# Kernel optimization log

Measured on AMD Instinct MI355X. Metric: run time of the kernel, lower is better.

## Reference

```python
import jax, jax.numpy as jnp
import numpy as np

N_NODES, N_EDGES, N_GRAPHS = 8192, 32768, 256
FXD, HEADS = 78, 10
D2 = FXD * HEADS  # 780
FF = 2048
L_MUT = 735
NF = 32
OUT_DIM = 128


def _ln(x, g, b, eps=1e-5):
    m = x.mean(-1, keepdims=True)
    v = ((x - m) ** 2).mean(-1, keepdims=True)
    return (x - m) * jax.lax.rsqrt(v + eps) * g + b


def _transformer(x, in_w, in_b, out_w, out_b, ln1_g, ln1_b, l1_w, l1_b, l2_w, l2_b, ln2_g, ln2_b):
    # post-LN TransformerEncoderLayer, nhead=1, seq = all N nodes, batch = 1 (eval: dropout off)
    E = x.shape[-1]
    q, k, v = jnp.split(x @ in_w.T + in_b, 3, axis=-1)
    a = jax.nn.softmax((q @ k.T) * (1.0 / np.sqrt(E)), axis=-1) @ v  # [N,N] scores
    x = _ln(x + a @ out_w.T + out_b, ln1_g, ln1_b)
    h = jax.nn.relu(x @ l1_w.T + l1_b) @ l2_w.T + l2_b
    return _ln(x + h, ln2_g, ln2_b)


def _gat(x, src, dst, w, a_src, a_dst, bias):
    # PyG GATConv, heads=10, concat=True, leaky 0.2, self loops already in src/dst
    N = x.shape[0]
    h = (x @ w.T).reshape(N, HEADS, FXD)
    asrc = (h * a_src).sum(-1)  # [N,H]
    adst = (h * a_dst).sum(-1)
    alpha = jax.nn.leaky_relu(asrc[src] + adst[dst], 0.2)  # [E,H]
    amax = jax.lax.stop_gradient(jax.ops.segment_max(alpha, dst, num_segments=N))
    ex = jnp.exp(alpha - amax[dst])
    coef = ex / (jax.ops.segment_sum(ex, dst, num_segments=N)[dst] + 1e-16)
    out = jax.ops.segment_sum(coef[:, :, None] * h[src], dst, num_segments=N)
    return out.reshape(N, HEADS * FXD) + bias


def _gcn(x, src, dst, w, b):
    # PyG GCNConv with self loops (already in src/dst), symmetric norm
    N = x.shape[0]
    deg = jax.ops.segment_sum(jnp.ones(dst.shape, x.dtype), dst, num_segments=N)
    dis = jnp.where(deg > 0, jax.lax.rsqrt(jnp.maximum(deg, 1.0)), 0.0)
    norm = dis[src] * dis[dst]
    return jax.ops.segment_sum(norm[:, None] * (x @ w.T)[src], dst, num_segments=N) + b


def _conv1d(x, w, b):
    y = jax.lax.conv_general_dilated(x, w, (1,), 'VALID', dimension_numbers=('NCH', 'OIH', 'NCH'))
    return y + b[None, :, None]


def _convT1d(x, w, b):
    # torch ConvTranspose1d weight [in,out,k] -> flipped [out,in,k], full padding
    k = w.shape[-1]
    ker = jnp.flip(w, -1).transpose(1, 0, 2)
    y = jax.lax.conv_general_dilated(x, ker, (1,), [(k - 1, k - 1)], dimension_numbers=('NCH', 'OIH', 'NCH'))
    return y + b[None, :, None]


def _maxpool1d(x, k):
    return jax.lax.reduce_window(x, -jnp.inf, jax.lax.max, (1, 1, k), (1, 1, k), 'VALID')


def _bn_eval(x, g, b, eps=1e-5):
    # eval-mode BatchNorm1d with fresh running stats (mean 0, var 1)
    return x * (g / np.sqrt(1.0 + eps))[None, :, None] + b[None, :, None]


def _forward(edge_index, batch, x, target_mut, t1_in_w, t1_in_b, t1_out_w, t1_out_b, t1_ln1_g, t1_ln1_b, t1_l1_w, t1_l1_b, t1_l2_w, t1_l2_b, t1_ln2_g, t1_ln2_b, gat_w, gat_asrc, gat_adst, gat_b, t2_in_w, t2_in_b, t2_out_w, t2_out_b, t2_ln1_g, t2_ln1_b, t2_l1_w, t2_l1_b, t2_l2_w, t2_l2_b, t2_ln2_g, t2_ln2_b, gcn_w, gcn_b, fcg1_w, fcg1_b, fcg2_w, fcg2_b, e1_w, e1_b, bn1_g, bn1_b, e2_w, e2_b, bn2_g, bn2_b, e3_w, e3_b, enc_lin_w, enc_lin_b, d3_w, d3_b, dbn2_g, dbn2_b, d2_w, d2_b, dbn1_g, dbn1_b, d1_w, d1_b, fc1_w, fc1_b, fc2_w, fc2_b, out_w, out_b):
    N = x.shape[0]
    xg = _transformer(x, t1_in_w, t1_in_b, t1_out_w, t1_out_b, t1_ln1_g, t1_ln1_b, t1_l1_w, t1_l1_b, t1_l2_w, t1_l2_b, t1_ln2_g, t1_ln2_b)
    loops = jnp.arange(N, dtype=edge_index.dtype)
    src = jnp.concatenate([edge_index[0], loops])
    dst = jnp.concatenate([edge_index[1], loops])
    xg = jax.nn.relu(_gat(xg, src, dst, gat_w, gat_asrc, gat_adst, gat_b))
    xg = _transformer(xg, t2_in_w, t2_in_b, t2_out_w, t2_out_b, t2_ln1_g, t2_ln1_b, t2_l1_w, t2_l1_b, t2_l2_w, t2_l2_b, t2_ln2_g, t2_ln2_b)
    xg = jax.nn.relu(_gcn(xg, src, dst, gcn_w, gcn_b))
    gm = jax.ops.segment_max(xg, batch, num_segments=N_GRAPHS)
    gm = jnp.where(jnp.isfinite(gm), gm, 0.0)
    cnt = jax.ops.segment_sum(jnp.ones((N,), xg.dtype), batch, num_segments=N_GRAPHS)
    ga = jax.ops.segment_sum(xg, batch, num_segments=N_GRAPHS) / jnp.maximum(cnt, 1.0)[:, None]
    xd = jnp.concatenate([gm, ga], axis=1)  # [B, 1560]
    xd = jax.nn.relu(xd @ fcg1_w.T + fcg1_b)
    xd = xd @ fcg2_w.T + fcg2_b  # [B, 128]
    # conv1d autoencoder on mutation profile
    t = target_mut[:, None, :]  # [B,1,735]
    e = jax.nn.leaky_relu(_bn_eval(_maxpool1d(_conv1d(t, e1_w, e1_b), 8), bn1_g, bn1_b))
    e = jax.nn.leaky_relu(_bn_eval(_maxpool1d(_conv1d(e, e2_w, e2_b), 7), bn2_g, bn2_b))
    e = _conv1d(e, e3_w, e3_b)  # [B,128,5]
    z = e.reshape(e.shape[0], -1) @ enc_lin_w.T + enc_lin_b  # [B,128]
    d = jnp.repeat(jax.nn.leaky_relu(_bn_eval(_convT1d(e, d3_w, d3_b), dbn2_g, dbn2_b)), 7, axis=-1)
    d = jnp.repeat(jax.nn.leaky_relu(_bn_eval(_convT1d(d, d2_w, d2_b), dbn1_g, dbn1_b)), 8, axis=-1)
    decode = _convT1d(d, d1_w, d1_b)  # [B,1,735]
    xc = jnp.concatenate([xd, z], axis=1)
    xc = jax.nn.relu(xc @ fc1_w.T + fc1_b)
    xc = jax.nn.relu(xc @ fc2_w.T + fc2_b)
    out = jax.nn.sigmoid(xc @ out_w.T + out_b)
    return (out, xd, decode)


def setup_inputs():
    key = jax.random.key(0)
    ks = iter(jax.random.split(key, 64))

    def rn(*shape):
        return jax.random.normal(next(ks), shape, jnp.float32) * 0.05

    inp = {}
    inp['x'] = jax.random.normal(next(ks), (N_NODES, FXD), jnp.float32)
    inp['edge_index'] = jax.random.randint(next(ks), (2, N_EDGES), 0, N_NODES)
    inp['batch'] = jnp.sort(jax.random.randint(next(ks), (N_NODES,), 0, N_GRAPHS))
    inp['target_mut'] = jax.random.normal(next(ks), (N_GRAPHS, L_MUT), jnp.float32)
    for p, E in (('t1', FXD), ('t2', D2)):
        inp[p + '_in_w'] = rn(3 * E, E); inp[p + '_in_b'] = jnp.zeros((3 * E,))
        inp[p + '_out_w'] = rn(E, E); inp[p + '_out_b'] = jnp.zeros((E,))
        inp[p + '_ln1_g'] = jnp.ones((E,)); inp[p + '_ln1_b'] = jnp.zeros((E,))
        inp[p + '_l1_w'] = rn(FF, E); inp[p + '_l1_b'] = jnp.zeros((FF,))
        inp[p + '_l2_w'] = rn(E, FF); inp[p + '_l2_b'] = jnp.zeros((E,))
        inp[p + '_ln2_g'] = jnp.ones((E,)); inp[p + '_ln2_b'] = jnp.zeros((E,))
    inp['gat_w'] = rn(D2, FXD); inp['gat_asrc'] = rn(HEADS, FXD); inp['gat_adst'] = rn(HEADS, FXD); inp['gat_b'] = jnp.zeros((D2,))
    inp['gcn_w'] = rn(D2, D2); inp['gcn_b'] = jnp.zeros((D2,))
    inp['fcg1_w'] = rn(1500, 2 * D2); inp['fcg1_b'] = jnp.zeros((1500,))
    inp['fcg2_w'] = rn(OUT_DIM, 1500); inp['fcg2_b'] = jnp.zeros((OUT_DIM,))
    inp['e1_w'] = rn(NF, 1, 8); inp['e1_b'] = jnp.zeros((NF,))
    inp['bn1_g'] = jnp.ones((NF,)); inp['bn1_b'] = jnp.zeros((NF,))
    inp['e2_w'] = rn(2 * NF, NF, 8); inp['e2_b'] = jnp.zeros((2 * NF,))
    inp['bn2_g'] = jnp.ones((2 * NF,)); inp['bn2_b'] = jnp.zeros((2 * NF,))
    inp['e3_w'] = rn(4 * NF, 2 * NF, 8); inp['e3_b'] = jnp.zeros((4 * NF,))
    inp['enc_lin_w'] = rn(OUT_DIM, 640); inp['enc_lin_b'] = jnp.zeros((OUT_DIM,))
    inp['d3_w'] = rn(4 * NF, 2 * NF, 8); inp['d3_b'] = jnp.zeros((2 * NF,))
    inp['dbn2_g'] = jnp.ones((2 * NF,)); inp['dbn2_b'] = jnp.zeros((2 * NF,))
    inp['d2_w'] = rn(2 * NF, NF, 8); inp['d2_b'] = jnp.zeros((NF,))
    inp['dbn1_g'] = jnp.ones((NF,)); inp['dbn1_b'] = jnp.zeros((NF,))
    inp['d1_w'] = rn(NF, 1, 8); inp['d1_b'] = jnp.zeros((1,))
    inp['fc1_w'] = rn(1024, 2 * OUT_DIM); inp['fc1_b'] = jnp.zeros((1024,))
    inp['fc2_w'] = rn(128, 1024); inp['fc2_b'] = jnp.zeros((128,))
    inp['out_w'] = rn(1, 128); inp['out_b'] = jnp.zeros((1,))
    return inp


def reference(x, edge_index, batch, target_mut, t1_in_w, t1_in_b, t1_out_w, t1_out_b, t1_ln1_g, t1_ln1_b, t1_l1_w, t1_l1_b, t1_l2_w, t1_l2_b, t1_ln2_g, t1_ln2_b, gat_w, gat_asrc, gat_adst, gat_b, t2_in_w, t2_in_b, t2_out_w, t2_out_b, t2_ln1_g, t2_ln1_b, t2_l1_w, t2_l1_b, t2_l2_w, t2_l2_b, t2_ln2_g, t2_ln2_b, gcn_w, gcn_b, fcg1_w, fcg1_b, fcg2_w, fcg2_b, e1_w, e1_b, bn1_g, bn1_b, e2_w, e2_b, bn2_g, bn2_b, e3_w, e3_b, enc_lin_w, enc_lin_b, d3_w, d3_b, dbn2_g, dbn2_b, d2_w, d2_b, dbn1_g, dbn1_b, d1_w, d1_b, fc1_w, fc1_b, fc2_w, fc2_b, out_w, out_b):
    return _forward(edge_index, batch, x, target_mut, t1_in_w, t1_in_b, t1_out_w, t1_out_b, t1_ln1_g, t1_ln1_b, t1_l1_w, t1_l1_b, t1_l2_w, t1_l2_b, t1_ln2_g, t1_ln2_b, gat_w, gat_asrc, gat_adst, gat_b, t2_in_w, t2_in_b, t2_out_w, t2_out_b, t2_ln1_g, t2_ln1_b, t2_l1_w, t2_l1_b, t2_l2_w, t2_l2_b, t2_ln2_g, t2_ln2_b, gcn_w, gcn_b, fcg1_w, fcg1_b, fcg2_w, fcg2_b, e1_w, e1_b, bn1_g, bn1_b, e2_w, e2_b, bn2_g, bn2_b, e3_w, e3_b, enc_lin_w, enc_lin_b, d3_w, d3_b, dbn2_g, dbn2_b, d2_w, d2_b, dbn1_g, dbn1_b, d1_w, d1_b, fc1_w, fc1_b, fc2_w, fc2_b, out_w, out_b)
```

## Files before the change

kernel.cpp:

```cpp
#include <hip/hip_runtime.h>
#include <math.h>

#define NN     8192
#define NEDGE  32768
#define NETOT  40960
#define NG     256
#define FXD_   78
#define NH     10
#define DD2    780
#define FFD    2048
#define LMUT   735

static inline int cdiv_i(long long a, int b){ return (int)((a + (long long)b - 1) / b); }
static inline int pad32(int x){ return (x + 31) & ~31; }

typedef __attribute__((ext_vector_type(8))) short bf16x8;
typedef __attribute__((ext_vector_type(4))) float f32x4;

static __device__ __forceinline__ unsigned short f2bf(float f){
    unsigned u = __float_as_uint(f);
    u += 0x7FFFu + ((u >> 16) & 1u);
    return (unsigned short)(u >> 16);
}

static __device__ __forceinline__ void gload16(const void* g, void* l){
    __builtin_amdgcn_global_load_lds((const __attribute__((address_space(1))) void*)g,
                                     (__attribute__((address_space(3))) void*)l, 16, 0, 0);
}

__global__ void fill_f32_k(float* __restrict__ p, float v, long long n){
    long long i = (long long)blockIdx.x * 256 + threadIdx.x;
    if (i < n) p[i] = v;
}
__global__ void fill_u32_k(unsigned* __restrict__ p, unsigned v, long long n){
    long long i = (long long)blockIdx.x * 256 + threadIdx.x;
    if (i < n) p[i] = v;
}

__global__ void cvt_pad_k(const float* __restrict__ src, unsigned short* __restrict__ dst,
                          long long n , int C, int lds_, int ldd)
{
    long long i = (long long)blockIdx.x * 256 + threadIdx.x;
    if (i >= n) return;
    int r = (int)(i / ldd), c = (int)(i % ldd);
    dst[i] = (c < C) ? f2bf(src[(size_t)r * lds_ + c]) : (unsigned short)0;
}

__global__ void tr_bf16_k(const unsigned short* __restrict__ src, unsigned short* __restrict__ dst,
                          int R, int C, int lds_, int ldd)
{
    __shared__ unsigned short t[32][33];
    int cb = blockIdx.x * 32, rb = blockIdx.y * 32;
    int tx = threadIdx.x & 31, ty = threadIdx.x >> 5;
#pragma unroll
    for (int i = 0; i < 4; ++i){
        int r = rb + ty + i * 8, c = cb + tx;
        t[ty + i * 8][tx] = (r < R && c < C) ? src[(size_t)r * lds_ + c] : (unsigned short)0;
    }
    __syncthreads();
#pragma unroll
    for (int i = 0; i < 4; ++i){
        int dr = cb + ty + i * 8, dc = rb + tx;
        if (dr < C && dc < R) dst[(size_t)dr * ldd + dc] = t[tx][ty + i * 8];
    }
}

__global__ void qkv_bias_k(const float* __restrict__ b3, float* __restrict__ out, int E, int Ep)
{
    int idx = blockIdx.x * 256 + threadIdx.x;
    if (idx >= 3 * Ep) return;
    int s = idx / Ep, c = idx % Ep;
    out[idx] = (c < E) ? b3[s * E + c] : 0.f;
}

__global__ void bias_add_k(float* __restrict__ X, const float* __restrict__ b, long long n, int cols)
{
    long long i = (long long)blockIdx.x * 256 + threadIdx.x;
    if (i < n) X[i] += b[i % cols];
}

template<int OUTC, int ACT, int SPLITK, int BROW, int BN>
__global__ __launch_bounds__(256) void mgemm_k(
    const unsigned short* __restrict__ A, const unsigned short* __restrict__ B,
    const float* __restrict__ bias, void* __restrict__ Cv,
    int M, int N, int Kp, int lda, int ldb, int ldc, int swz)
{
    constexpr int NFJ   = BN / 32;
    constexpr int TILEA = 128 * 32;
    constexpr int TILEB = BN * 32;
    __shared__ unsigned short As[2 * TILEA];
    __shared__ unsigned short Bs[2 * TILEB];
    const int tid = threadIdx.x;
    const int lane = tid & 63, wid = tid >> 6;
    const int r16 = lane & 15, q = lane >> 4;
    const int wr = (wid >> 1) * 64, wc = (wid & 1) * (BN / 2);

    const int gx = gridDim.x, gy = gridDim.y;
    const int nwg = gx * gy;
    int orig = swz ? ((int)blockIdx.x * gy + (int)blockIdx.y)
                   : ((int)blockIdx.y * gx + (int)blockIdx.x);
    int q8 = nwg >> 3, r8 = nwg & 7;
    int xcd = orig & 7, kk8 = orig >> 3;
    int wgid = (xcd < r8 ? xcd * (q8 + 1) : r8 * (q8 + 1) + (xcd - r8) * q8) + kk8;
    int bx, by;
    if (swz){ by = wgid % gy; bx = wgid / gy; }
    else    { bx = wgid % gx; by = wgid / gx; }
    const int row0 = by * 128, col0 = bx * BN;

    int kbeg = 0, kend = Kp;
    if (SPLITK > 1){
        int nt_ = Kp >> 5, cpt = (nt_ + SPLITK - 1) / SPLITK;
        kbeg = (int)blockIdx.z * cpt * 32;
        kend = min(Kp, kbeg + cpt * 32);
    }

    const int c0 = wid * 128 + lane;
    const int r0a = c0 >> 2, k0a = (c0 & 3) << 3;
    const size_t gA0 = (size_t)min(row0 + r0a, M - 1) * lda + k0a;
    const size_t gA1 = (size_t)min(row0 + r0a + 16, M - 1) * lda + k0a;
    unsigned short* lA = As + wid * 1024;
    size_t gB0 = 0, gB1 = 0;
    unsigned short* lB;
    if (BN == 128){
        gB0 = (size_t)min(col0 + r0a, N - 1) * ldb + k0a;
        gB1 = (size_t)min(col0 + r0a + 16, N - 1) * ldb + k0a;
        lB = Bs + wid * 1024;
    } else {
        const int cb = wid * 64 + lane;
        const int rb_ = cb >> 2, kb_ = (cb & 3) << 3;
        gB0 = (size_t)min(col0 + rb_, N - 1) * ldb + kb_;
        lB = Bs + wid * 512;
    }

    f32x4 acc[4][NFJ];
#pragma unroll
    for (int i = 0; i < 4; ++i)
#pragma unroll
        for (int j = 0; j < NFJ; ++j){ f32x4 z = {0.f, 0.f, 0.f, 0.f}; acc[i][j] = z; }

    const int nt = (kend - kbeg) >> 5;
    if (nt > 0){
        gload16(A + gA0 + kbeg, lA);
        gload16(A + gA1 + kbeg, lA + 512);
        gload16(B + gB0 + kbeg, lB);
        if (BN == 128) gload16(B + gB1 + kbeg, lB + 512);
        __syncthreads();
        int cur = 0;
        for (int t = 0; t < nt; ++t){
            const int k0 = kbeg + (t << 5);
            if (t + 1 < nt){
                const int kn = k0 + 32, nb = cur ^ 1;
                gload16(A + gA0 + kn, lA + nb * TILEA);
                gload16(A + gA1 + kn, lA + nb * TILEA + 512);
                gload16(B + gB0 + kn, lB + nb * TILEB);
                if (BN == 128) gload16(B + gB1 + kn, lB + nb * TILEB + 512);
            }
            const unsigned short* Ab = As + cur * TILEA;
            const unsigned short* Bb = Bs + cur * TILEB;
            bf16x8 af[4], bfv[NFJ];
#pragma unroll
            for (int f = 0; f < 4; ++f)
                af[f] = *(const bf16x8*)(Ab + (size_t)(wr + f * 16 + r16) * 32 + (q << 3));
#pragma unroll
            for (int f = 0; f < NFJ; ++f)
                bfv[f] = *(const bf16x8*)(Bb + (size_t)(wc + f * 16 + r16) * 32 + (q << 3));
#pragma unroll
            for (int fi = 0; fi < 4; ++fi)
#pragma unroll
                for (int fj = 0; fj < NFJ; ++fj)
                    acc[fi][fj] = __builtin_amdgcn_mfma_f32_16x16x32_bf16(af[fi], bfv[fj], acc[fi][fj], 0, 0, 0);
            __syncthreads();
            cur ^= 1;
        }
    }

#pragma unroll
    for (int fi = 0; fi < 4; ++fi){
#pragma unroll
        for (int j = 0; j < 4; ++j){
            int r = row0 + wr + fi * 16 + q * 4 + j;
            if (r >= M) continue;
#pragma unroll
            for (int fj = 0; fj < NFJ; ++fj){
                int c = col0 + wc + fj * 16 + r16;
                if (c >= N) continue;
                float v = acc[fi][fj][j];
                if (SPLITK > 1){
                    atomicAdd((float*)Cv + (size_t)r * ldc + c, v);
                } else {
                    if (bias) v += BROW ? bias[r] : bias[c];
                    if (ACT == 1) v = fmaxf(v, 0.f);
                    if (ACT == 2) v = 1.f / (1.f + expf(-v));
                    if (OUTC == 0) ((float*)Cv)[(size_t)r * ldc + c] = v;
                    else ((unsigned short*)Cv)[(size_t)r * ldc + c] = f2bf(v);
                }
            }
        }
    }
}

template<int OUTC, int ACT, int SPLITK, int BROW, int BN>
static void mgemm(hipStream_t s, const unsigned short* A, const unsigned short* B,
                  const float* bias, void* C, int M, int N, int Kp,
                  int lda, int ldb, int ldc, int swz)
{
    dim3 g(cdiv_i(N, BN), cdiv_i(M, 128), SPLITK);
    mgemm_k<OUTC, ACT, SPLITK, BROW, BN><<<g, 256, 0, s>>>(A, B, bias, C, M, N, Kp, lda, ldb, ldc, swz);
}

__global__ __launch_bounds__(256) void softmax_bf16_k(unsigned short* __restrict__ SP, float scale)
{
    __shared__ float red[8];
    const int tid = threadIdx.x;
    uint4* prow = (uint4*)(SP + (size_t)blockIdx.x * NN);
    float v[32];
    float mx = -3.4e38f;
#pragma unroll
    for (int c = 0; c < 4; ++c){
        uint4 t = prow[c * 256 + tid];
        const unsigned* u = (const unsigned*)&t;
#pragma unroll
        for (int j = 0; j < 4; ++j){
            float lo = __uint_as_float(u[j] << 16) * scale;
            float hi = __uint_as_float(u[j] & 0xFFFF0000u) * scale;
            v[c * 8 + j * 2]     = lo;
            v[c * 8 + j * 2 + 1] = hi;
            mx = fmaxf(mx, fmaxf(lo, hi));
        }
    }
#pragma unroll
    for (int off = 32; off; off >>= 1) mx = fmaxf(mx, __shfl_xor(mx, off, 64));
    if ((tid & 63) == 0) red[tid >> 6] = mx;
    __syncthreads();
    mx = fmaxf(fmaxf(red[0], red[1]), fmaxf(red[2], red[3]));
    float sum = 0.f;
#pragma unroll
    for (int i = 0; i < 32; ++i){ v[i] = expf(v[i] - mx); sum += v[i]; }
#pragma unroll
    for (int off = 32; off; off >>= 1) sum += __shfl_xor(sum, off, 64);
    if ((tid & 63) == 0) red[4 + (tid >> 6)] = sum;
    __syncthreads();
    float inv = 1.f / (red[4] + red[5] + red[6] + red[7]);
#pragma unroll
    for (int c = 0; c < 4; ++c){
        uint4 t;
        unsigned* u = (unsigned*)&t;
#pragma unroll
        for (int j = 0; j < 4; ++j){
            unsigned lo = f2bf(v[c * 8 + j * 2] * inv);
            unsigned hi = f2bf(v[c * 8 + j * 2 + 1] * inv);
            u[j] = lo | (hi << 16);
        }
        prow[c * 256 + tid] = t;
    }
}

__global__ __launch_bounds__(256) void add_ln_k(
    const float* __restrict__ X, const float* __restrict__ Y, const float* __restrict__ ybias,
    const float* __restrict__ g, const float* __restrict__ b,
    float* __restrict__ out, unsigned short* __restrict__ obf, int E, int Ep)
{
    __shared__ float s1[256], s2[256];
    const int tid = threadIdx.x;
    long long base = (long long)blockIdx.x * E;
    float vals[4];
    float sum = 0.f, sq = 0.f;
    int i = 0;
    for (int c = tid; c < Ep; c += 256, ++i){
        float v = 0.f;
        if (c < E){
            v = X[base + c] + Y[base + c];
            if (ybias) v += ybias[c];
            sum += v; sq += v * v;
        }
        vals[i] = v;
    }
    s1[tid] = sum; s2[tid] = sq; __syncthreads();
    for (int s = 128; s; s >>= 1){
        if (tid < s){ s1[tid] += s1[tid + s]; s2[tid] += s2[tid + s]; }
        __syncthreads();
    }
    float mean = s1[0] / (float)E;
    float var = s2[0] / (float)E - mean * mean;
    if (var < 0.f) var = 0.f;
    float inv = 1.f / sqrtf(var + 1e-5f);
    i = 0;
    for (int c = tid; c < Ep; c += 256, ++i){
        if (c < E){
            float o = (vals[i] - mean) * inv * g[c] + b[c];
            out[base + c] = o;
            if (obf) obf[(size_t)blockIdx.x * Ep + c] = f2bf(o);
        } else if (obf) obf[(size_t)blockIdx.x * Ep + c] = 0;
    }
}

static __device__ __forceinline__ unsigned enc_f(float x){
    unsigned u = __float_as_uint(x);
    return (u & 0x80000000u) ? ~u : (u | 0x80000000u);
}
static __device__ __forceinline__ float dec_f(unsigned u){
    return (u & 0x80000000u) ? __uint_as_float(u & 0x7fffffffu) : __uint_as_float(~u);
}
static __device__ __forceinline__ void edge_sd(const int* __restrict__ ei, int e, int& s, int& d){
    if (e < NEDGE){ s = ei[e]; d = ei[NEDGE + e]; }
    else { s = e - NEDGE; d = e - NEDGE; }
}

__global__ void gat_srcdst_k(const float* __restrict__ h, const float* __restrict__ aw_src,
                             const float* __restrict__ aw_dst, float* __restrict__ asrc,
                             float* __restrict__ adst)
{
    int idx = blockIdx.x * 256 + threadIdx.x;
    if (idx >= NN * NH) return;
    int n = idx / NH, hh = idx % NH;
    const float* hp = h + (long long)n * DD2 + hh * FXD_;
    const float* ws = aw_src + hh * FXD_;
    const float* wd = aw_dst + hh * FXD_;
    float s1 = 0.f, s2 = 0.f;
    for (int f = 0; f < FXD_; ++f){ float v = hp[f]; s1 += v * ws[f]; s2 += v * wd[f]; }
    asrc[idx] = s1; adst[idx] = s2;
}

__global__ void gat_alpha_k(const int* __restrict__ ei, const float* __restrict__ asrc,
                            const float* __restrict__ adst, float* __restrict__ alpha,
                            unsigned* __restrict__ amax)
{
    int idx = blockIdx.x * 256 + threadIdx.x;
    if (idx >= NETOT * NH) return;
    int e = idx / NH, hh = idx % NH;
    int s, d; edge_sd(ei, e, s, d);
    float a = asrc[s * NH + hh] + adst[d * NH + hh];
    a = (a > 0.f) ? a : 0.2f * a;
    alpha[idx] = a;
    atomicMax(&amax[d * NH + hh], enc_f(a));
}

__global__ void gat_expsum_k(const int* __restrict__ ei, float* __restrict__ alpha,
                             const unsigned* __restrict__ amax, float* __restrict__ denom)
{
    int idx = blockIdx.x * 256 + threadIdx.x;
    if (idx >= NETOT * NH) return;
    int e = idx / NH, hh = idx % NH;
    int s, d; edge_sd(ei, e, s, d);
    float m = dec_f(amax[d * NH + hh]);
    float ex = expf(alpha[idx] - m);
    alpha[idx] = ex;
    atomicAdd(&denom[d * NH + hh], ex);
}

__global__ void deg_count_k(const int* __restrict__ ei, int* __restrict__ deg)
{
    int e = blockIdx.x * 256 + threadIdx.x;
    if (e >= NETOT) return;
    int s, d; edge_sd(ei, e, s, d);
    atomicAdd(&deg[d], 1);
}

__global__ __launch_bounds__(256) void csr_off_k(const int* __restrict__ deg,
                                                 int* __restrict__ off, int* __restrict__ cur)
{
    __shared__ int pref[257];
    const int tid = threadIdx.x;
    int loc[32];
    int base = tid * 32, sum = 0;
#pragma unroll
    for (int i = 0; i < 32; ++i){ loc[i] = sum; sum += deg[base + i]; }
    __shared__ int part[256];
    part[tid] = sum; __syncthreads();
    if (tid == 0){
        pref[0] = 0;
        for (int i = 0; i < 256; ++i) pref[i + 1] = pref[i] + part[i];
    }
    __syncthreads();
    int p0 = pref[tid];
#pragma unroll
    for (int i = 0; i < 32; ++i){ off[base + i] = p0 + loc[i]; cur[base + i] = p0 + loc[i]; }
    if (tid == 0) off[NN] = pref[256];
}

__global__ void csr_fill_k(const int* __restrict__ ei, int* __restrict__ cur,
                           int* __restrict__ csr_s, int* __restrict__ csr_e)
{
    int e = blockIdx.x * 256 + threadIdx.x;
    if (e >= NETOT) return;
    int s, d; edge_sd(ei, e, s, d);
    int pos = atomicAdd(&cur[d], 1);
    csr_s[pos] = s; csr_e[pos] = e;
}

__global__ __launch_bounds__(256) void gat_gather_k(
    const int* __restrict__ off, const int* __restrict__ csr_s, const int* __restrict__ csr_e,
    const float* __restrict__ ex, const float* __restrict__ denom,
    const float* __restrict__ hfeat, float* __restrict__ out)
{
    const int d = blockIdx.x, tid = threadIdx.x;
    const int beg = off[d], end = off[d + 1];
    for (int f = tid; f < DD2; f += 256){
        int hh = f / FXD_;
        float acc = 0.f;
        for (int p = beg; p < end; ++p)
            acc += ex[csr_e[p] * NH + hh] * hfeat[(size_t)csr_s[p] * DD2 + f];
        out[(size_t)d * DD2 + f] = acc / (denom[d * NH + hh] + 1e-16f);
    }
}

__global__ __launch_bounds__(256) void gcn_gather_k(
    const int* __restrict__ off, const int* __restrict__ csr_s,
    const float* __restrict__ dis, const float* __restrict__ xw, float* __restrict__ out)
{
    const int d = blockIdx.x, tid = threadIdx.x;
    const int beg = off[d], end = off[d + 1];
    const float dd_ = dis[d];
    for (int f = tid; f < DD2; f += 256){
        float acc = 0.f;
        for (int p = beg; p < end; ++p){
            int s = csr_s[p];
            acc += dis[s] * xw[(size_t)s * DD2 + f];
        }
        out[(size_t)d * DD2 + f] = acc * dd_;
    }
}

__global__ void bias_relu_k(float* __restrict__ X, const float* __restrict__ b,
                            unsigned short* __restrict__ obf, int rows, int cols, int ldp)
{
    long long i = (long long)blockIdx.x * 256 + threadIdx.x;
    if (i >= (long long)rows * ldp) return;
    int r = (int)(i / ldp), c = (int)(i % ldp);
    if (c < cols){
        float v = X[(size_t)r * cols + c] + b[c];
        v = v > 0.f ? v : 0.f;
        X[(size_t)r * cols + c] = v;
        if (obf) obf[i] = f2bf(v);
    } else if (obf) obf[i] = 0;
}

__global__ void dis_k(const int* __restrict__ deg, float* __restrict__ dis)
{
    int n = blockIdx.x * 256 + threadIdx.x;
    if (n >= NN) return;
    float d = (float)deg[n];
    dis[n] = (d > 0.f) ? 1.f / sqrtf(fmaxf(d, 1.f)) : 0.f;
}

__global__ void seg_start_k(const int* __restrict__ batch, int* __restrict__ start)
{
    int n = blockIdx.x * 256 + threadIdx.x;
    if (n >= NN) return;
    int b = batch[n];
    int bp = (n == 0) ? -1 : batch[n - 1];
    for (int g = bp + 1; g <= b; ++g) start[g] = n;
    if (n == NN - 1){
        for (int g = b + 1; g <= NG; ++g) start[g] = NN;
    }
}

__global__ __launch_bounds__(256) void pool_seg_k(const float* __restrict__ xg,
                                                  const int* __restrict__ start,
                                                  unsigned short* __restrict__ xdb)
{
    const int g = blockIdx.x, tid = threadIdx.x;
    const int s0 = start[g], s1 = start[g + 1];
    const float inv = 1.f / fmaxf((float)(s1 - s0), 1.f);
    for (int f = tid; f < DD2; f += 256){
        float mx = 0.f, sm = 0.f;
        for (int n = s0; n < s1; ++n){
            float v = xg[(size_t)n * DD2 + f];
            mx = fmaxf(mx, v); sm += v;
        }
        xdb[(size_t)g * 1568 + f] = f2bf(mx);
        xdb[(size_t)g * 1568 + DD2 + f] = f2bf(sm * inv);
    }
    if (tid < 8) xdb[(size_t)g * 1568 + 1560 + tid] = 0;
}

#define BN_SCALE 0.9999950000374996f

__global__ __launch_bounds__(256) void enc1_b(const float* __restrict__ tm, const float* __restrict__ w,
                                              const float* __restrict__ bias, const float* __restrict__ bng,
                                              const float* __restrict__ bnb, float* __restrict__ out)
{
    __shared__ float xs[736];
    __shared__ float ws[256], bs[32], gs[32], b2[32];
    const int g = blockIdx.x, tid = threadIdx.x;
    for (int i = tid; i < 735; i += 256) xs[i] = tm[(size_t)g * LMUT + i];
    ws[tid] = w[tid];
    if (tid < 32){ bs[tid] = bias[tid]; gs[tid] = bng[tid]; b2[tid] = bnb[tid]; }
    __syncthreads();
    for (int idx = tid; idx < 32 * 91; idx += 256){
        int o = idx / 91, t = idx % 91;
        float mx = -3.4e38f;
        for (int p = 0; p < 8; ++p){
            float s = bs[o];
#pragma unroll
            for (int k = 0; k < 8; ++k) s += xs[t * 8 + p + k] * ws[o * 8 + k];
            mx = fmaxf(mx, s);
        }
        float v = mx * gs[o] * BN_SCALE + b2[o];
        out[(size_t)g * 2912 + idx] = v > 0.f ? v : 0.01f * v;
    }
}

__global__ void i2c_enc2_k(const float* __restrict__ in, unsigned short* __restrict__ A){
    int idx = blockIdx.x * 256 + threadIdx.x;
    if (idx >= NG * 84 * 256) return;
    int col = idx & 255, row = idx >> 8;
    int g = row / 84, u = row % 84;
    int i = col >> 3, k = col & 7;
    A[idx] = f2bf(in[(size_t)g * 2912 + i * 91 + u + k]);
}
__global__ void post_enc2_k(const float* __restrict__ G, const float* __restrict__ b,
                            const float* __restrict__ bng, const float* __restrict__ bnb,
                            float* __restrict__ out){
    int idx = blockIdx.x * 256 + threadIdx.x;
    if (idx >= NG * 768) return;
    int t = idx % 12, o = (idx / 12) & 63, g = idx / 768;
    float mx = -3.4e38f;
#pragma unroll
    for (int p = 0; p < 7; ++p) mx = fmaxf(mx, G[(size_t)(g * 84 + t * 7 + p) * 64 + o]);
    float v = (mx + b[o]) * bng[o] * BN_SCALE + bnb[o];
    out[(size_t)g * 768 + o * 12 + t] = v > 0.f ? v : 0.01f * v;
}
__global__ void i2c_enc3_k(const float* __restrict__ in, unsigned short* __restrict__ A){
    int idx = blockIdx.x * 256 + threadIdx.x;
    if (idx >= NG * 5 * 512) return;
    int col = idx & 511, row = idx >> 9;
    int g = row / 5, t = row % 5;
    int i2 = col >> 3, k = col & 7;
    A[idx] = f2bf(in[(size_t)g * 768 + i2 * 12 + t + k]);
}
__global__ void post_enc3_k(const float* __restrict__ G, const float* __restrict__ b,
                            float* __restrict__ e3o, unsigned short* __restrict__ obf){
    int idx = blockIdx.x * 256 + threadIdx.x;
    if (idx >= NG * 640) return;
    int t = idx % 5, o = (idx / 5) & 127, g = idx / 640;
    float v = G[(size_t)(g * 5 + t) * 128 + o] + b[o];
    e3o[(size_t)g * 640 + o * 5 + t] = v;
    obf[(size_t)g * 640 + o * 5 + t] = f2bf(v);
}
__global__ void wshuf_k(const float* __restrict__ src, unsigned short* __restrict__ dst, int I, int O){
    int idx = blockIdx.x * 256 + threadIdx.x;
    if (idx >= I * O * 8) return;
    int o = idx / (I * 8), rem = idx % (I * 8);
    int i = rem >> 3, j = rem & 7;
    dst[idx] = f2bf(src[(size_t)(i * O + o) * 8 + j]);
}
__global__ void i2c_dec3_k(const float* __restrict__ e3o, unsigned short* __restrict__ A){
    int idx = blockIdx.x * 256 + threadIdx.x;
    if (idx >= NG * 12 * 1024) return;
    int col = idx & 1023, row = idx >> 10;
    int g = row / 12, t = row % 12;
    int i2 = col >> 3, j = col & 7;
    int tt = t - j;
    A[idx] = (tt >= 0 && tt < 5) ? f2bf(e3o[(size_t)g * 640 + i2 * 5 + tt]) : (unsigned short)0;
}
__global__ void post_dec3_k(const float* __restrict__ G, const float* __restrict__ b,
                            const float* __restrict__ bng, const float* __restrict__ bnb,
                            float* __restrict__ dd3){
    int idx = blockIdx.x * 256 + threadIdx.x;
    if (idx >= NG * 768) return;
    int t = idx % 12, o = (idx / 12) & 63, g = idx / 768;
    float v = (G[(size_t)(g * 12 + t) * 64 + o] + b[o]) * bng[o] * BN_SCALE + bnb[o];
    dd3[(size_t)g * 768 + o * 12 + t] = v > 0.f ? v : 0.01f * v;
}
__global__ void i2c_dec2_k(const float* __restrict__ dd3, unsigned short* __restrict__ A){
    int idx = blockIdx.x * 256 + threadIdx.x;
    if (idx >= NG * 91 * 512) return;
    int col = idx & 511, row = idx >> 9;
    int g = row / 91, t = row % 91;
    int i2 = col >> 3, j = col & 7;
    int tt = t - j;
    A[idx] = (tt >= 0 && tt < 84) ? f2bf(dd3[(size_t)g * 768 + i2 * 12 + tt / 7]) : (unsigned short)0;
}
__global__ void post_dec2_k(const float* __restrict__ G, const float* __restrict__ b,
                            const float* __restrict__ bng, const float* __restrict__ bnb,
                            float* __restrict__ dd2){
    int idx = blockIdx.x * 256 + threadIdx.x;
    if (idx >= NG * 2912) return;
    int t = idx % 91, o = (idx / 91) & 31, g = idx / 2912;
    float v = (G[(size_t)(g * 91 + t) * 32 + o] + b[o]) * bng[o] * BN_SCALE + bnb[o];
    dd2[(size_t)g * 2912 + o * 91 + t] = v > 0.f ? v : 0.01f * v;
}

__global__ __launch_bounds__(256) void dec1_b(const float* __restrict__ dd2, const float* __restrict__ w,
                                              const float* __restrict__ bias, float* __restrict__ out)
{
    __shared__ float d2s[32][91];
    __shared__ float ws[256];
    const int g = blockIdx.x, tid = threadIdx.x;
    const int t0 = (int)blockIdx.y * 245;
    for (int i = tid; i < 32 * 91; i += 256) d2s[i / 91][i % 91] = dd2[(size_t)g * 2912 + i];
    ws[tid] = w[tid];
    __syncthreads();
    if (tid < 245){
        int t = t0 + tid;
        int id8[8]; bool ok[8];
#pragma unroll
        for (int j = 0; j < 8; ++j){
            int tt = t - j;
            ok[j] = (tt >= 0 && tt < 728);
            id8[j] = ok[j] ? (tt >> 3) : 0;
        }
        float s = bias[0];
        for (int i2 = 0; i2 < 32; ++i2){
            const float* wp = ws + i2 * 8;
            float a = 0.f;
#pragma unroll
            for (int j = 0; j < 8; ++j) if (ok[j]) a += d2s[i2][id8[j]] * wp[j];
            s += a;
        }
        out[(size_t)g * 735 + t] = s;
    }
}

__global__ void concat_xc_k(const float* __restrict__ xd, const float* __restrict__ z,
                            unsigned short* __restrict__ xcb)
{
    int idx = blockIdx.x * 256 + threadIdx.x;
    if (idx >= NG * 256) return;
    int g = idx >> 8, c = idx & 255;
    xcb[idx] = f2bf((c < 128) ? xd[g * 128 + c] : z[g * 128 + (c - 128)]);
}

extern "C" void kernel_launch(void* const* d_in, const int* in_sizes, int n_in,
                              void* d_out, int out_size, void* d_ws, size_t ws_size,
                              hipStream_t stream)
{
    (void)in_sizes; (void)n_in; (void)out_size;

    const float* x      = (const float*)d_in[0];
    const int*   ei     = (const int*)  d_in[1];
    const int*   batch  = (const int*)  d_in[2];
    const float* tmut   = (const float*)d_in[3];
    const float* t1w[12]; for (int i = 0; i < 12; ++i) t1w[i] = (const float*)d_in[4 + i];
    const float* t2w[12]; for (int i = 0; i < 12; ++i) t2w[i] = (const float*)d_in[16 + i];
    const float* gat_w    = (const float*)d_in[28];
    const float* gat_asrc = (const float*)d_in[29];
    const float* gat_adst = (const float*)d_in[30];
    const float* gat_b    = (const float*)d_in[31];
    const float* gcn_w  = (const float*)d_in[32];
    const float* gcn_b  = (const float*)d_in[33];
    const float* fcg1_w = (const float*)d_in[34];
    const float* fcg1_b = (const float*)d_in[35];
    const float* fcg2_w = (const float*)d_in[36];
    const float* fcg2_b = (const float*)d_in[37];
    const float* e1_w = (const float*)d_in[38]; const float* e1_b = (const float*)d_in[39];
    const float* bn1_g = (const float*)d_in[40]; const float* bn1_b = (const float*)d_in[41];
    const float* e2_w = (const float*)d_in[42]; const float* e2_b = (const float*)d_in[43];
    const float* bn2_g = (const float*)d_in[44]; const float* bn2_b = (const float*)d_in[45];
    const float* e3_w = (const float*)d_in[46]; const float* e3_b = (const float*)d_in[47];
    const float* enc_w = (const float*)d_in[48]; const float* enc_b = (const float*)d_in[49];
    const float* d3_w = (const float*)d_in[50]; const float* d3_b = (const float*)d_in[51];
    const float* dbn2_g = (const float*)d_in[52]; const float* dbn2_b = (const float*)d_in[53];
    const float* d2_w = (const float*)d_in[54]; const float* d2_b = (const float*)d_in[55];
    const float* dbn1_g = (const float*)d_in[56]; const float* dbn1_b = (const float*)d_in[57];
    const float* d1_w = (const float*)d_in[58]; const float* d1_b = (const float*)d_in[59];
    const float* fc1_w = (const float*)d_in[60]; const float* fc1_b = (const float*)d_in[61];
    const float* fc2_w = (const float*)d_in[62]; const float* fc2_b = (const float*)d_in[63];
    const float* outw = (const float*)d_in[64]; const float* outb = (const float*)d_in[65];

    float *A1, *A2, *A3, *A4, *X1f, *QBIASf;
    unsigned short *XB, *QKVb, *Vt, *HbPb;
    unsigned short *WQKVb, *WOUTb, *WL1b, *WL2b, *WGb, *WGCNb, *WFCG1b, *WFCG2b,
                   *WENCb, *WFC1b, *WFC2b, *WOUTWb, *XD16, *FG1b, *E3b, *XCb, *FH1b, *FH2b, *Wcvb;
    float *asrc, *adst, *alpha, *denom, *dis, *c1p, *c2p, *e3o, *zz, *dd3, *dd2b;
    unsigned *amax; int *deg, *seg, *csr_off, *csr_cur, *csr_s, *csr_e;

    auto carve = [&](long long RB) -> size_t {
        char* wp_ = (char*)d_ws;
        auto alc = [&](size_t bytes) -> char* {
            char* p = wp_;
            wp_ += (bytes + 255) & ~(size_t)255;
            return p;
        };
        A1 = (float*)alc((size_t)NN * DD2 * 4);
        A2 = (float*)alc((size_t)NN * DD2 * 4);
        A3 = (float*)alc((size_t)NN * DD2 * 4);
        A4 = (float*)alc((size_t)NN * DD2 * 4);
        X1f = (float*)alc((size_t)NN * FXD_ * 4);
        XB   = (unsigned short*)alc((size_t)NN * 800 * 2);
        QKVb = (unsigned short*)alc((size_t)NN * 2400 * 2);
        Vt   = (unsigned short*)alc((size_t)800 * NN * 2);
        size_t hb = (size_t)NN * FFD * 2, pb = (size_t)RB * NN * 2;
        HbPb = (unsigned short*)alc(hb > pb ? hb : pb);
        WQKVb = (unsigned short*)alc((size_t)2400 * 800 * 2);
        QBIASf= (float*)alc((size_t)2400 * 4);
        WOUTb = (unsigned short*)alc((size_t)780 * 800 * 2);
        WL1b  = (unsigned short*)alc((size_t)2048 * 800 * 2);
        WL2b  = (unsigned short*)alc((size_t)780 * 2048 * 2);
        WGb   = (unsigned short*)alc((size_t)780 * 96 * 2);
        WGCNb = (unsigned short*)alc((size_t)780 * 800 * 2);
        WFCG1b= (unsigned short*)alc((size_t)1500 * 1568 * 2);
        WFCG2b= (unsigned short*)alc((size_t)128 * 1504 * 2);
        WENCb = (unsigned short*)alc((size_t)128 * 640 * 2);
        WFC1b = (unsigned short*)alc((size_t)1024 * 256 * 2);
        WFC2b = (unsigned short*)alc((size_t)128 * 1024 * 2);
        WOUTWb= (unsigned short*)alc((size_t)128 * 2);
        Wcvb  = (unsigned short*)alc((size_t)128 * 1024 * 2);
        XD16  = (unsigned short*)alc((size_t)NG * 1568 * 2);
        FG1b  = (unsigned short*)alc((size_t)NG * 1504 * 2);
        E3b   = (unsigned short*)alc((size_t)NG * 640 * 2);
        XCb   = (unsigned short*)alc((size_t)NG * 256 * 2);
        FH1b  = (unsigned short*)alc((size_t)NG * 1024 * 2);
        FH2b  = (unsigned short*)alc((size_t)NG * 128 * 2);
        asrc = (float*)alc((size_t)NN * NH * 4);
        adst = (float*)alc((size_t)NN * NH * 4);
        alpha= (float*)alc((size_t)NETOT * NH * 4);
        amax = (unsigned*)alc((size_t)NN * NH * 4);
        denom= (float*)alc((size_t)NN * NH * 4);
        deg  = (int*)alc((size_t)NN * 4);
        dis  = (float*)alc((size_t)NN * 4);
        seg  = (int*)alc((size_t)(NG + 1) * 4);
        csr_off = (int*)alc((size_t)(NN + 1) * 4);
        csr_cur = (int*)alc((size_t)NN * 4);
        csr_s   = (int*)alc((size_t)NETOT * 4);
        csr_e   = (int*)alc((size_t)NETOT * 4);
        c1p  = (float*)alc((size_t)NG * 32 * 91 * 4);
        c2p  = (float*)alc((size_t)NG * 64 * 12 * 4);
        e3o  = (float*)alc((size_t)NG * 128 * 5 * 4);
        zz   = (float*)alc((size_t)NG * 128 * 4);
        dd3  = (float*)alc((size_t)NG * 64 * 12 * 4);
        dd2b = (float*)alc((size_t)NG * 32 * 91 * 4);
        return (size_t)(wp_ - (char*)d_ws);
    };

    long long RB = 512;
    const long long cands[3] = {2048, 1024, 512};
    for (int i = 0; i < 3; ++i){ if (carve(cands[i]) <= ws_size){ RB = cands[i]; break; } }
    carve(RB);
    unsigned short* Pb = HbPb;
    unsigned short* AIM = HbPb;

    float* out0   = (float*)d_out;
    float* xd_out = (float*)d_out + NG;
    float* decode = (float*)d_out + NG + NG * 128;

    auto cvt = [&](const float* src, unsigned short* dst, int R, int C, int lds_, int ldd){
        long long n = (long long)R * ldd;
        cvt_pad_k<<<cdiv_i(n, 256), 256, 0, stream>>>(src, dst, n, C, lds_, ldd);
    };
    auto zero16 = [&](unsigned short* p, long long nshorts){
        fill_u32_k<<<cdiv_i(nshorts / 2, 256), 256, 0, stream>>>((unsigned*)p, 0u, nshorts / 2);
    };
    auto zerof = [&](float* p, long long n){
        fill_f32_k<<<cdiv_i(n, 256), 256, 0, stream>>>(p, 0.f, n);
    };

    auto run_tf = [&](const float* xin, const float* const* W, float* outp, int E){
        const int Ep = pad32(E), E3p = 3 * Ep;
        float scale = (float)(1.0 / sqrt((double)E));
        zero16(WQKVb, (long long)E3p * Ep);
        for (int s = 0; s < 3; ++s)
            cvt(W[0] + (size_t)s * E * E, WQKVb + (size_t)s * Ep * Ep, E, E, E, Ep);
        qkv_bias_k<<<cdiv_i(E3p, 256), 256, 0, stream>>>(W[1], QBIASf, E, Ep);
        mgemm<1,0,1,0,128>(stream, XB, WQKVb, QBIASf, QKVb, NN, E3p, Ep, Ep, Ep, E3p, 0);
        {
            dim3 g(cdiv_i(E, 32), cdiv_i(NN, 32));
            tr_bf16_k<<<g, 256, 0, stream>>>(QKVb + 2 * Ep, Vt, NN, E, E3p, NN);
        }
        zerof(A4, (long long)NN * E);
        for (long long r0 = 0; r0 < NN; r0 += RB){
            mgemm<1,0,1,0,128>(stream, QKVb + (size_t)r0 * E3p, QKVb + Ep, nullptr, Pb,
                               (int)RB, NN, Ep, E3p, E3p, NN, 1);
            softmax_bf16_k<<<(int)RB, 256, 0, stream>>>(Pb, scale);
            if (E == FXD_)
                mgemm<0,0,8,0,64>(stream, Pb, Vt, nullptr, A4 + (size_t)r0 * E,
                                  (int)RB, E, NN, NN, NN, E, 0);
            else
                mgemm<0,0,4,0,64>(stream, Pb, Vt, nullptr, A4 + (size_t)r0 * E,
                                  (int)RB, E, NN, NN, NN, E, 0);
        }
        cvt(A4, XB, NN, E, E, Ep);
        cvt(W[2], WOUTb, E, E, E, Ep);
        mgemm<0,0,1,0,64>(stream, XB, WOUTb, W[3], A2, NN, E, Ep, Ep, Ep, E, 0);
        add_ln_k<<<NN, 256, 0, stream>>>(xin, A2, nullptr, W[4], W[5], A3, XB, E, Ep);
        cvt(W[6], WL1b, FFD, E, E, Ep);
        mgemm<1,1,1,0,128>(stream, XB, WL1b, W[7], HbPb, NN, FFD, Ep, Ep, Ep, FFD, 0);
        cvt(W[8], WL2b, E, FFD, FFD, FFD);
        mgemm<0,0,1,0,64>(stream, HbPb, WL2b, W[9], A2, NN, E, FFD, FFD, FFD, E, 0);
        add_ln_k<<<NN, 256, 0, stream>>>(A3, A2, nullptr, W[10], W[11], outp, XB, E, Ep);
    };

    cvt(x, XB, NN, FXD_, FXD_, 96);
    run_tf(x, t1w, X1f, FXD_);

    fill_u32_k<<<cdiv_i(NN, 256), 256, 0, stream>>>((unsigned*)deg, 0u, NN);
    deg_count_k<<<cdiv_i(NETOT, 256), 256, 0, stream>>>(ei, deg);
    csr_off_k<<<1, 256, 0, stream>>>(deg, csr_off, csr_cur);
    csr_fill_k<<<cdiv_i(NETOT, 256), 256, 0, stream>>>(ei, csr_cur, csr_s, csr_e);
    seg_start_k<<<cdiv_i(NN, 256), 256, 0, stream>>>(batch, seg);

    cvt(gat_w, WGb, DD2, FXD_, FXD_, 96);
    mgemm<0,0,1,0,64>(stream, XB, WGb, nullptr, A2, NN, DD2, 96, 96, 96, DD2, 0);
    gat_srcdst_k<<<cdiv_i((long long)NN * NH, 256), 256, 0, stream>>>(A2, gat_asrc, gat_adst, asrc, adst);
    fill_u32_k<<<cdiv_i((long long)NN * NH, 256), 256, 0, stream>>>(amax, 0x007FFFFFu, (long long)NN * NH);
    zerof(denom, (long long)NN * NH);
    gat_alpha_k<<<cdiv_i((long long)NETOT * NH, 256), 256, 0, stream>>>(ei, asrc, adst, alpha, amax);
    gat_expsum_k<<<cdiv_i((long long)NETOT * NH, 256), 256, 0, stream>>>(ei, alpha, amax, denom);
    gat_gather_k<<<NN, 256, 0, stream>>>(csr_off, csr_s, csr_e, alpha, denom, A2, A1);
    bias_relu_k<<<cdiv_i((long long)NN * 800, 256), 256, 0, stream>>>(A1, gat_b, XB, NN, DD2, 800);

    run_tf(A1, t2w, A1, DD2);

    dis_k<<<cdiv_i(NN, 256), 256, 0, stream>>>(deg, dis);
    cvt(gcn_w, WGCNb, DD2, DD2, DD2, 800);
    mgemm<0,0,1,0,64>(stream, XB, WGCNb, nullptr, A2, NN, DD2, 800, 800, 800, DD2, 0);
    gcn_gather_k<<<NN, 256, 0, stream>>>(csr_off, csr_s, dis, A2, A3);
    bias_relu_k<<<cdiv_i((long long)NN * DD2, 256), 256, 0, stream>>>(A3, gcn_b, nullptr, NN, DD2, DD2);

    pool_seg_k<<<NG, 256, 0, stream>>>(A3, seg, XD16);
    cvt(fcg1_w, WFCG1b, 1500, 1560, 1560, 1568);
    zerof(A2, (long long)NG * 1500);
    mgemm<0,0,8,0,64>(stream, XD16, WFCG1b, nullptr, A2, NG, 1500, 1568, 1568, 1568, 1500, 0);
    bias_relu_k<<<cdiv_i((long long)NG * 1504, 256), 256, 0, stream>>>(A2, fcg1_b, FG1b, NG, 1500, 1504);
    cvt(fcg2_w, WFCG2b, 128, 1500, 1500, 1504);
    zerof(xd_out, (long long)NG * 128);
    mgemm<0,0,16,0,128>(stream, FG1b, WFCG2b, nullptr, xd_out, NG, 128, 1504, 1504, 1504, 128, 0);
    bias_add_k<<<cdiv_i((long long)NG * 128, 256), 256, 0, stream>>>(xd_out, fcg2_b, (long long)NG * 128, 128);

    enc1_b<<<NG, 256, 0, stream>>>(tmut, e1_w, e1_b, bn1_g, bn1_b, c1p);
    i2c_enc2_k<<<cdiv_i((long long)NG * 84 * 256, 256), 256, 0, stream>>>(c1p, AIM);
    cvt(e2_w, Wcvb, 64, 256, 256, 256);
    mgemm<0,0,1,0,64>(stream, AIM, Wcvb, nullptr, A2, NG * 84, 64, 256, 256, 256, 64, 0);
    post_enc2_k<<<cdiv_i((long long)NG * 768, 256), 256, 0, stream>>>(A2, e2_b, bn2_g, bn2_b, c2p);
    i2c_enc3_k<<<cdiv_i((long long)NG * 5 * 512, 256), 256, 0, stream>>>(c2p, AIM);
    cvt(e3_w, Wcvb, 128, 512, 512, 512);
    zerof(A2, (long long)NG * 5 * 128);
    mgemm<0,0,4,0,128>(stream, AIM, Wcvb, nullptr, A2, NG * 5, 128, 512, 512, 512, 128, 0);
    post_enc3_k<<<cdiv_i((long long)NG * 640, 256), 256, 0, stream>>>(A2, e3_b, e3o, E3b);
    cvt(enc_w, WENCb, 128, 640, 640, 640);
    mgemm<0,0,1,0,128>(stream, E3b, WENCb, enc_b, zz, NG, 128, 640, 640, 640, 128, 0);

    wshuf_k<<<cdiv_i(128 * 64 * 8, 256), 256, 0, stream>>>(d3_w, Wcvb, 128, 64);
    i2c_dec3_k<<<cdiv_i((long long)NG * 12 * 1024, 256), 256, 0, stream>>>(e3o, AIM);
    zerof(A2, (long long)NG * 12 * 64);
    mgemm<0,0,4,0,64>(stream, AIM, Wcvb, nullptr, A2, NG * 12, 64, 1024, 1024, 1024, 64, 0);
    post_dec3_k<<<cdiv_i((long long)NG * 768, 256), 256, 0, stream>>>(A2, d3_b, dbn2_g, dbn2_b, dd3);
    wshuf_k<<<cdiv_i(64 * 32 * 8, 256), 256, 0, stream>>>(d2_w, Wcvb, 64, 32);
    i2c_dec2_k<<<cdiv_i((long long)NG * 91 * 512, 256), 256, 0, stream>>>(dd3, AIM);
    mgemm<0,0,1,0,64>(stream, AIM, Wcvb, nullptr, A2, NG * 91, 32, 512, 512, 512, 32, 0);
    post_dec2_k<<<cdiv_i((long long)NG * 2912, 256), 256, 0, stream>>>(A2, d2_b, dbn1_g, dbn1_b, dd2b);
    { dim3 g(NG, 3); dec1_b<<<g, 256, 0, stream>>>(dd2b, d1_w, d1_b, decode); }

    concat_xc_k<<<cdiv_i((long long)NG * 256, 256), 256, 0, stream>>>(xd_out, zz, XCb);
    cvt(fc1_w, WFC1b, 1024, 256, 256, 256);
    mgemm<1,1,1,0,128>(stream, XCb, WFC1b, fc1_b, FH1b, NG, 1024, 256, 256, 256, 1024, 0);
    cvt(fc2_w, WFC2b, 128, 1024, 1024, 1024);
    zerof(A3, (long long)NG * 128);
    mgemm<0,0,8,0,128>(stream, FH1b, WFC2b, nullptr, A3, NG, 128, 1024, 1024, 1024, 128, 0);
    bias_relu_k<<<cdiv_i((long long)NG * 128, 256), 256, 0, stream>>>(A3, fc2_b, FH2b, NG, 128, 128);
    cvt(outw, WOUTWb, 1, 128, 128, 128);
    mgemm<0,2,1,0,64>(stream, FH2b, WOUTWb, outb, out0, NG, 1, 128, 128, 128, 1, 0);
}
```

Baseline: 1.766 ms.

## Fuse softmax exp into score GEMM and get row sums via a ones column

```diff
diff --git a/kernel.cpp b/kernel.cpp
--- a/kernel.cpp
+++ b/kernel.cpp
@@ -46,6 +46,15 @@
     dst[i] = (c < C) ? f2bf(src[(size_t)r * lds_ + c]) : (unsigned short)0;
 }
 
+__global__ void norm_cvt_k(const float* __restrict__ A4, unsigned short* __restrict__ XB,
+                           int E, int Ep)
+{
+    long long i = (long long)blockIdx.x * 256 + threadIdx.x;
+    if (i >= (long long)NN * Ep) return;
+    int r = (int)(i / Ep), c = (int)(i % Ep);
+    XB[i] = (c < E) ? f2bf(A4[(size_t)r * Ep + c] / A4[(size_t)r * Ep + E]) : (unsigned short)0;
+}
+
 __global__ void tr_bf16_k(const unsigned short* __restrict__ src, unsigned short* __restrict__ dst,
                           int R, int C, int lds_, int ldd)
 {
@@ -83,7 +92,7 @@
 __global__ __launch_bounds__(256) void mgemm_k(
     const unsigned short* __restrict__ A, const unsigned short* __restrict__ B,
     const float* __restrict__ bias, void* __restrict__ Cv,
-    int M, int N, int Kp, int lda, int ldb, int ldc, int swz)
+    int M, int N, int Kp, int lda, int ldb, int ldc, int swz, float escale)
 {
     constexpr int NFJ   = BN / 32;
     constexpr int TILEA = 128 * 32;
@@ -191,6 +200,7 @@
                     if (bias) v += BROW ? bias[r] : bias[c];
                     if (ACT == 1) v = fmaxf(v, 0.f);
                     if (ACT == 2) v = 1.f / (1.f + expf(-v));
+                    if (ACT == 3) v = expf(v * escale);
                     if (OUTC == 0) ((float*)Cv)[(size_t)r * ldc + c] = v;
                     else ((unsigned short*)Cv)[(size_t)r * ldc + c] = f2bf(v);
                 }
@@ -202,57 +212,10 @@
 template<int OUTC, int ACT, int SPLITK, int BROW, int BN>
 static void mgemm(hipStream_t s, const unsigned short* A, const unsigned short* B,
                   const float* bias, void* C, int M, int N, int Kp,
-                  int lda, int ldb, int ldc, int swz)
+                  int lda, int ldb, int ldc, int swz, float escale = 1.f)
 {
     dim3 g(cdiv_i(N, BN), cdiv_i(M, 128), SPLITK);
-    mgemm_k<OUTC, ACT, SPLITK, BROW, BN><<<g, 256, 0, s>>>(A, B, bias, C, M, N, Kp, lda, ldb, ldc, swz);
-}
-
-__global__ __launch_bounds__(256) void softmax_bf16_k(unsigned short* __restrict__ SP, float scale)
-{
-    __shared__ float red[8];
-    const int tid = threadIdx.x;
-    uint4* prow = (uint4*)(SP + (size_t)blockIdx.x * NN);
-    float v[32];
-    float mx = -3.4e38f;
-#pragma unroll
-    for (int c = 0; c < 4; ++c){
-        uint4 t = prow[c * 256 + tid];
-        const unsigned* u = (const unsigned*)&t;
-#pragma unroll
-        for (int j = 0; j < 4; ++j){
-            float lo = __uint_as_float(u[j] << 16) * scale;
-            float hi = __uint_as_float(u[j] & 0xFFFF0000u) * scale;
-            v[c * 8 + j * 2]     = lo;
-            v[c * 8 + j * 2 + 1] = hi;
-            mx = fmaxf(mx, fmaxf(lo, hi));
-        }
-    }
-#pragma unroll
-    for (int off = 32; off; off >>= 1) mx = fmaxf(mx, __shfl_xor(mx, off, 64));
-    if ((tid & 63) == 0) red[tid >> 6] = mx;
-    __syncthreads();
-    mx = fmaxf(fmaxf(red[0], red[1]), fmaxf(red[2], red[3]));
-    float sum = 0.f;
-#pragma unroll
-    for (int i = 0; i < 32; ++i){ v[i] = expf(v[i] - mx); sum += v[i]; }
-#pragma unroll
-    for (int off = 32; off; off >>= 1) sum += __shfl_xor(sum, off, 64);
-    if ((tid & 63) == 0) red[4 + (tid >> 6)] = sum;
-    __syncthreads();
-    float inv = 1.f / (red[4] + red[5] + red[6] + red[7]);
-#pragma unroll
-    for (int c = 0; c < 4; ++c){
-        uint4 t;
-        unsigned* u = (unsigned*)&t;
-#pragma unroll
-        for (int j = 0; j < 4; ++j){
-            unsigned lo = f2bf(v[c * 8 + j * 2] * inv);
-            unsigned hi = f2bf(v[c * 8 + j * 2 + 1] * inv);
-            u[j] = lo | (hi << 16);
-        }
-        prow[c * 256 + tid] = t;
-    }
+    mgemm_k<OUTC, ACT, SPLITK, BROW, BN><<<g, 256, 0, s>>>(A, B, bias, C, M, N, Kp, lda, ldb, ldc, swz, escale);
 }
 
 __global__ __launch_bounds__(256) void add_ln_k(
@@ -676,11 +639,11 @@
         A1 = (float*)alc((size_t)NN * DD2 * 4);
         A2 = (float*)alc((size_t)NN * DD2 * 4);
         A3 = (float*)alc((size_t)NN * DD2 * 4);
-        A4 = (float*)alc((size_t)NN * DD2 * 4);
+        A4 = (float*)alc((size_t)NN * 800 * 4);
         X1f = (float*)alc((size_t)NN * FXD_ * 4);
         XB   = (unsigned short*)alc((size_t)NN * 800 * 2);
         QKVb = (unsigned short*)alc((size_t)NN * 2400 * 2);
-        Vt   = (unsigned short*)alc((size_t)800 * NN * 2);
+        Vt   = (unsigned short*)alc((size_t)801 * NN * 2);
         size_t hb = (size_t)NN * FFD * 2, pb = (size_t)RB * NN * 2;
         HbPb = (unsigned short*)alc(hb > pb ? hb : pb);
         WQKVb = (unsigned short*)alc((size_t)2400 * 800 * 2);
@@ -757,20 +720,21 @@
         {
             dim3 g(cdiv_i(E, 32), cdiv_i(NN, 32));
             tr_bf16_k<<<g, 256, 0, stream>>>(QKVb + 2 * Ep, Vt, NN, E, E3p, NN);
-        }
-        zerof(A4, (long long)NN * E);
+            fill_u32_k<<<cdiv_i(NN / 2, 256), 256, 0, stream>>>((unsigned*)(Vt + (size_t)E * NN),
+                                                                0x3F803F80u, NN / 2);
+        }
+        zerof(A4, (long long)NN * Ep);
         for (long long r0 = 0; r0 < NN; r0 += RB){
-            mgemm<1,0,1,0,128>(stream, QKVb + (size_t)r0 * E3p, QKVb + Ep, nullptr, Pb,
-                               (int)RB, NN, Ep, E3p, E3p, NN, 1);
-            softmax_bf16_k<<<(int)RB, 256, 0, stream>>>(Pb, scale);
+            mgemm<1,3,1,0,128>(stream, QKVb + (size_t)r0 * E3p, QKVb + Ep, nullptr, Pb,
+                               (int)RB, NN, Ep, E3p, E3p, NN, 1, scale);
             if (E == FXD_)
-                mgemm<0,0,8,0,64>(stream, Pb, Vt, nullptr, A4 + (size_t)r0 * E,
-                                  (int)RB, E, NN, NN, NN, E, 0);
+                mgemm<0,0,8,0,64>(stream, Pb, Vt, nullptr, A4 + (size_t)r0 * Ep,
+                                  (int)RB, E + 1, NN, NN, NN, Ep, 0);
             else
-                mgemm<0,0,4,0,64>(stream, Pb, Vt, nullptr, A4 + (size_t)r0 * E,
-                                  (int)RB, E, NN, NN, NN, E, 0);
-        }
-        cvt(A4, XB, NN, E, E, Ep);
+                mgemm<0,0,4,0,64>(stream, Pb, Vt, nullptr, A4 + (size_t)r0 * Ep,
+                                  (int)RB, E + 1, NN, NN, NN, Ep, 0);
+        }
+        norm_cvt_k<<<cdiv_i((long long)NN * Ep, 256), 256, 0, stream>>>(A4, XB, E, Ep);
         cvt(W[2], WOUTb, E, E, E, Ep);
         mgemm<0,0,1,0,64>(stream, XB, WOUTb, W[3], A2, NN, E, Ep, Ep, Ep, E, 0);
         add_ln_k<<<NN, 256, 0, stream>>>(xin, A2, nullptr, W[4], W[5], A3, XB, E, Ep);
```

After: 1.643 ms. 1.08x faster.
